# Kernel optimization log

Hardware: AMD Instinct MI355X
Metric: run time of the kernel (lower is better)

Reference implementation:

```python
import math
import jax, jax.numpy as jnp
import numpy as np

# Gemma4Audio config constants
HID = 1024
H = 8
D = HID // H            # 128
CHUNK = 12              # attention_chunk_size
PAST = 13 - 1           # max_past_horizon = context_left - 1
FUT = 0                 # max_future_horizon = context_right
CTX = CHUNK + PAST + FUT  # 24
SOFTCAP = 50.0
Q_SCALE = D ** (-0.5) / math.log(2)
K_SCALE = math.log(1.0 + math.e) / math.log(2)


def setup_inputs() -> dict:
    key = jax.random.key(0)
    ks = jax.random.split(key, 8)
    B, S = 4, 6144
    P = CTX + 1  # 25 relative positions
    std = HID ** (-0.5)
    return {
        "hidden_states": jax.random.normal(ks[0], (B, S, HID), jnp.float32),
        "position_embeddings": jax.random.normal(ks[1], (P, HID), jnp.float32),
        "Wq": jax.random.normal(ks[2], (HID, HID), jnp.float32) * std,
        "Wk": jax.random.normal(ks[3], (HID, HID), jnp.float32) * std,
        "Wv": jax.random.normal(ks[4], (HID, HID), jnp.float32) * std,
        "Wpost": jax.random.normal(ks[5], (HID, HID), jnp.float32) * std,
        "Wrel": jax.random.normal(ks[6], (HID, HID), jnp.float32) * std,
        "per_dim_scale": jnp.zeros((D,), jnp.float32),  # torch init: zeros
    }


def _extract_block_context(x, num_blocks):
    # x: [B, S, H, D] -> [B, num_blocks, CTX, H, D]
    xp = jnp.pad(x, ((0, 0), (PAST, FUT + CHUNK - 1), (0, 0), (0, 0)))
    idx = jnp.arange(num_blocks)[:, None] * CHUNK + jnp.arange(CTX)[None, :]
    return xp[:, idx]  # gather along seq axis


def _rel_shift(x):
    # x: [B, H, nb, CHUNK, P] -> [B, H, nb, CHUNK, CTX]
    B, Hh, nb, bs, pos_len = x.shape
    x = jnp.pad(x, ((0, 0), (0, 0), (0, 0), (0, 0), (0, CTX + 1 - pos_len)))
    x = x.reshape(B, Hh, nb, bs * (CTX + 1))[..., : bs * CTX]
    return x.reshape(B, Hh, nb, bs, CTX)


def reference(hidden_states, position_embeddings, Wq, Wk, Wv, Wpost, Wrel, per_dim_scale):
    B, S, _ = hidden_states.shape
    nb = (S + CHUNK - 1) // CHUNK
    pad = nb * CHUNK - S

    # Projections (ClippableLinear clamps are +/-inf at init -> identity)
    q = (hidden_states @ Wq.T).reshape(B, S, H, D)
    k = (hidden_states @ Wk.T).reshape(B, S, H, D)
    v = (hidden_states @ Wv.T).reshape(B, S, H, D)

    q = q * (Q_SCALE * jax.nn.softplus(per_dim_scale))  # per-dim scaled queries
    k = k * K_SCALE

    # [B, nb, CHUNK, H, D]
    q_blocked = jnp.pad(q, ((0, 0), (0, pad), (0, 0), (0, 0))).reshape(B, nb, CHUNK, H, D)
    k_ctx = _extract_block_context(k, nb)  # [B, nb, CTX, H, D]
    v_ctx = _extract_block_context(v, nb)

    # content score: [B, H, nb, CHUNK, CTX]
    matrix_ac = jnp.einsum('bnchd,bnkhd->bhnck', q_blocked, k_ctx)

    # relative position score
    rel_k = (position_embeddings @ Wrel.T).reshape(-1, H, D)  # [P, H, D]
    matrix_bd = jnp.einsum('bnchd,phd->bhncp', q_blocked, rel_k)
    matrix_bd = _rel_shift(matrix_bd)  # [B, H, nb, CHUNK, CTX]

    logits = matrix_ac + matrix_bd
    logits = jnp.tanh(logits / SOFTCAP) * SOFTCAP  # softcap
    attn = jax.nn.softmax(logits, axis=-1)

    out = jnp.einsum('bhnck,bnkhd->bnchd', attn, v_ctx)
    out = out.reshape(B, nb * CHUNK, H * D)[:, :S]
    return out @ Wpost.T
```

## Files before the change

kernel.cpp:

```cpp
#include <hip/hip_runtime.h>
#include <hip/hip_bf16.h>
#include <math.h>

typedef unsigned short ushort_t;
typedef __attribute__((ext_vector_type(8))) short short8;
typedef __attribute__((ext_vector_type(4))) short s4v;
typedef __attribute__((ext_vector_type(4))) float float4v;

#define HID 1024
#define NH 8
#define DH 128
#define CHUNK 12
#define PAST 12
#define CTX 24
#define NPOS 25
#define QKVW 3072

__device__ __forceinline__ float bf2f(ushort_t b){
  union{unsigned int u; float f;} x; x.u = ((unsigned int)b)<<16; return x.f;
}
__device__ __forceinline__ ushort_t f2bf(float f){
  union{float f; unsigned int u;} x; x.f = f;
  unsigned int u = x.u;
  unsigned int r = u + 0x7fffu + ((u>>16)&1u);
  return (ushort_t)(r>>16);
}

__device__ __forceinline__ void gload16(const ushort_t* g, ushort_t* l){
  __builtin_amdgcn_global_load_lds(
      (const __attribute__((address_space(1))) unsigned int*)g,
      (__attribute__((address_space(3))) unsigned int*)l,
      16, 0, 0);
}

__global__ __launch_bounds__(256) void cvt_all(
    const float* __restrict__ hs, const float* __restrict__ Wq,
    const float* __restrict__ Wk, const float* __restrict__ Wv,
    const float* __restrict__ Wp, ushort_t* __restrict__ hsb,
    ushort_t* __restrict__ Wcat, ushort_t* __restrict__ Wpb, int nhs4)
{
  const int W4 = 262144;
  const int total = nhs4 + 4*W4;
  for (int i = blockIdx.x*256 + threadIdx.x; i < total; i += gridDim.x*256){
    const float4v* src; s4v* dst; int off;
    if (i < nhs4){ src = (const float4v*)hs; dst = (s4v*)hsb; off = i; }
    else {
      int j = i - nhs4; int seg = j >> 18; off = j & (W4-1);
      src = (const float4v*)(seg==0?Wq:seg==1?Wk:seg==2?Wv:Wp);
      dst = (seg<3) ? ((s4v*)Wcat) + (size_t)seg*W4 : (s4v*)Wpb;
    }
    float4v v = src[off];
    s4v o;
#pragma unroll
    for (int j2=0;j2<4;j2++) o[j2] = (short)f2bf(v[j2]);
    dst[off] = o;
  }
}

template<int MODE, int OUTF>
__global__ __launch_bounds__(256) void gemm3(
    const ushort_t* __restrict__ A, const ushort_t* __restrict__ W,
    void* __restrict__ Cv, int M, int N, int K,
    const float* __restrict__ pds, float qsc, float ksc)
{
  const int nwg  = gridDim.x;
  const int orig = blockIdx.x;
  const int qch  = nwg >> 3, rch = nwg & 7;
  const int xcd  = orig & 7, idx = orig >> 3;
  const int bid  = (xcd < rch ? xcd*(qch+1) : rch*(qch+1) + (xcd-rch)*qch) + idx;

  const int NT = N >> 7;
  const int m0 = (bid / NT) * 128;
  const int n0 = (bid % NT) * 128;

  const int tid  = threadIdx.x;
  const int w    = tid >> 6, lane = tid & 63;
  const int wm   = w >> 1, wn = w & 1;
  const int lr   = lane & 15;
  const int lg   = lane >> 4;

  __shared__ ushort_t slab[6*128*32];
  ushort_t* a0 = slab;                 ushort_t* b0 = slab + 128*32;
  ushort_t* a1 = slab + 2*128*32;      ushort_t* b1 = slab + 3*128*32;
  ushort_t* a2 = slab + 4*128*32;      ushort_t* b2 = slab + 5*128*32;

  float4v acc[4][4];
#pragma unroll
  for (int i=0;i<4;i++)
#pragma unroll
    for (int j=0;j<4;j++) acc[i][j] = (float4v)0.0f;

  const int sr = lane >> 2;
  const int sc = (lane & 3) * 8;

  const ushort_t* Ab0 = A + (size_t)(m0 + w*16      + sr)*K + sc;
  const ushort_t* Ab1 = A + (size_t)(m0 + 64 + w*16 + sr)*K + sc;
  const ushort_t* Bb0 = W + (size_t)(n0 + w*16      + sr)*K + sc;
  const ushort_t* Bb1 = W + (size_t)(n0 + 64 + w*16 + sr)*K + sc;

#define STAGE(Abuf, Bbuf, kt) do {                    \
    gload16(Ab0 + (kt), &(Abuf)[(w*16)*32]);          \
    gload16(Ab1 + (kt), &(Abuf)[(64 + w*16)*32]);     \
    gload16(Bb0 + (kt), &(Bbuf)[(w*16)*32]);          \
    gload16(Bb1 + (kt), &(Bbuf)[(64 + w*16)*32]);     \
  } while(0)

#define COMPUTE(Abuf, Bbuf) do {                                             \
    short8 afr[4], bfr[4];                                                   \
    _Pragma("unroll")                                                        \
    for (int i=0;i<4;i++) afr[i] = *(const short8*)&(Abuf)[(wm*64 + i*16 + lr)*32 + lg*8]; \
    _Pragma("unroll")                                                        \
    for (int j=0;j<4;j++) bfr[j] = *(const short8*)&(Bbuf)[(wn*64 + j*16 + lr)*32 + lg*8]; \
    __builtin_amdgcn_s_setprio(1);                                           \
    _Pragma("unroll")                                                        \
    for (int i=0;i<4;i++)                                                    \
      _Pragma("unroll")                                                      \
      for (int j=0;j<4;j++)                                                  \
        acc[i][j] = __builtin_amdgcn_mfma_f32_16x16x32_bf16(afr[i], bfr[j], acc[i][j], 0,0,0); \
    __builtin_amdgcn_s_setprio(0);                                           \
  } while(0)

  const int nt = K >> 5;
  STAGE(a0, b0, 0);
  STAGE(a1, b1, 32);

  for (int t = 0; t < nt; ++t){
    if (t == nt-1) asm volatile("s_waitcnt vmcnt(0)" ::: "memory");
    else           asm volatile("s_waitcnt vmcnt(4)" ::: "memory");
    asm volatile("s_barrier" ::: "memory");
    if (t+2 < nt) STAGE(a2, b2, (t+2)*32);
    COMPUTE(a0, b0);
    ushort_t* ta = a0; a0 = a1; a1 = a2; a2 = ta;
    ushort_t* tb = b0; b0 = b1; b1 = b2; b2 = tb;
  }
#undef STAGE
#undef COMPUTE

  __syncthreads();

  if (OUTF == 0){
#pragma unroll
    for (int j=0;j<4;j++){
      const int col = wn*64 + j*16 + lr;
      float scale = 1.0f;
      if (MODE==1){
        const int gcol = n0 + col;
        if (gcol < 1024){ float p = pds[gcol & (DH-1)]; scale = qsc * log1pf(expf(p)); }
        else if (gcol < 2048) scale = ksc;
      }
#pragma unroll
      for (int i=0;i<4;i++){
        const int row = wm*64 + i*16 + lg*4;
#pragma unroll
        for (int r=0;r<4;r++)
          slab[(row + r)*128 + col] = f2bf(acc[i][j][r] * scale);
      }
    }
    __syncthreads();
    ushort_t* Crow = (ushort_t*)Cv + (size_t)m0*N + n0;
    const int rr = tid >> 4, sl = (tid & 15)*8;
#pragma unroll
    for (int it=0; it<8; ++it){
      const int row = it*16 + rr;
      *(short8*)&Crow[(size_t)row*N + sl] = *(const short8*)&slab[row*128 + sl];
    }
  } else {
    float* smf = (float*)slab;
    float* Crow = (float*)Cv + (size_t)m0*N + n0;
#pragma unroll
    for (int h2=0; h2<2; ++h2){
      __syncthreads();
      if (wm == h2){
#pragma unroll
        for (int j=0;j<4;j++){
          const int col = wn*64 + j*16 + lr;
#pragma unroll
          for (int i=0;i<4;i++){
            const int row = i*16 + lg*4;
#pragma unroll
            for (int r=0;r<4;r++)
              smf[(row + r)*128 + col] = acc[i][j][r];
          }
        }
      }
      __syncthreads();
      const int rr = tid >> 5, half = ((tid >> 4) & 1)*64, sl = (tid & 15)*4;
#pragma unroll
      for (int it=0; it<8; ++it){
        const int row = it*8 + rr;
        *(float4v*)&Crow[(size_t)(h2*64 + row)*N + half + sl] =
            *(const float4v*)&smf[row*128 + half + sl];
      }
    }
  }
}

__global__ __launch_bounds__(256) void relk2(
    const float* __restrict__ pe, const float* __restrict__ Wrel,
    ushort_t* __restrict__ rel)
{
  int g = blockIdx.x*256 + threadIdx.x;
  int idx = g >> 1, par = g & 1;
  if (idx >= NPOS*HID) return;
  int p = idx >> 10, n = idx & 1023;
  const float* a = pe + p*HID + par*512;
  const float* w = Wrel + (size_t)n*HID + par*512;
  float s = 0.f;
  for (int k=0;k<512;k+=4){
    float4v av = *(const float4v*)(a+k);
    float4v wv = *(const float4v*)(w+k);
#pragma unroll
    for (int u=0;u<4;u++) s += av[u]*wv[u];
  }
  s += __shfl_xor(s, 1, 64);
  if (!par) rel[idx] = f2bf(s);
}

__global__ __launch_bounds__(256) void attn_kernel(
  const ushort_t* __restrict__ qkv, const ushort_t* __restrict__ rel,
  ushort_t* __restrict__ o, int S)
{
  const int n0 = blockIdx.x * 4;
  const int b  = blockIdx.y, h = blockIdx.z;
  const int tid = threadIdx.x;
  const size_t bS = (size_t)b * S;

  __shared__ ushort_t lds[24800];
  ushort_t* ks = lds;
  ushort_t* vt = lds + 9248;
  float*    sB = (float*)(lds + 17952);
  ushort_t* rs = lds + 20448;
  float*    sA = (float*)(lds + 20448);

  const int base = n0*CHUNK - PAST;
  {
    const int r0 = tid >> 4;
    const int c0 = (tid & 15) * 8;
    for (int r = r0; r < 68; r += 16){
      int s = base + r;
      short8 kv = (short8)0, vv = (short8)0;
      if (r < 60 && s >= 0 && s < S){
        kv = *(const short8*)&qkv[(bS + s)*QKVW + 1024 + h*DH + c0];
        vv = *(const short8*)&qkv[(bS + s)*QKVW + 2048 + h*DH + c0];
      }
      *(short8*)&ks[r*136 + c0] = kv;
#pragma unroll
      for (int u=0;u<8;u++) vt[(c0+u)*68 + r] = (ushort_t)vv[u];
    }
    for (int r = r0; r < 32; r += 16){
      short8 rv = (short8)0;
      if (r < NPOS) rv = *(const short8*)&rel[r*HID + h*DH + c0];
      *(short8*)&rs[r*136 + c0] = rv;
    }
  }
  __syncthreads();

  const int w    = tid >> 6;
  const int lane = tid & 63;
  const int lr   = lane & 15;
  const int lg   = lane >> 4;

  float*    sAw = sA + w*312;
  float*    sBw = sB + w*312;
  ushort_t* Ppw = lds + w*640;

  int qrow = (n0 + w)*CHUNK + lr;
  if (qrow >= S) qrow = S - 1;
  const ushort_t* qp = qkv + (bS + qrow)*QKVW + h*DH + lg*8;
  short8 qf[4];
#pragma unroll
  for (int ks2=0; ks2<4; ks2++) qf[ks2] = *(const short8*)(qp + ks2*32);

#pragma unroll
  for (int t0=0; t0<2; t0++){
    float4v acc = (float4v)0.0f;
#pragma unroll
    for (int ks2=0; ks2<4; ks2++){
      short8 rf = *(const short8*)&rs[(t0*16 + lr)*136 + ks2*32 + lg*8];
      acc = __builtin_amdgcn_mfma_f32_16x16x32_bf16(qf[ks2], rf, acc, 0,0,0);
    }
    const int p = t0*16 + lr;
#pragma unroll
    for (int reg=0; reg<4; reg++){
      int cr = lg*4 + reg;
      if (cr < CHUNK && p < NPOS) sBw[cr*26 + p] = acc[reg];
    }
  }
  __syncthreads();

#pragma unroll
  for (int t0=0; t0<2; t0++){
    float4v acc = (float4v)0.0f;
#pragma unroll
    for (int ks2=0; ks2<4; ks2++){
      short8 kf = *(const short8*)&ks[(w*CHUNK + t0*16 + lr)*136 + ks2*32 + lg*8];
      acc = __builtin_amdgcn_mfma_f32_16x16x32_bf16(qf[ks2], kf, acc, 0,0,0);
    }
    const int t = t0*16 + lr;
#pragma unroll
    for (int reg=0; reg<4; reg++){
      int cr = lg*4 + reg;
      if (cr < CHUNK && t < CTX) sAw[cr*26 + t] = acc[reg];
    }
  }
  __syncthreads();

  if (lane < CHUNK) *(short8*)&Ppw[lane*40 + 24] = (short8)0;

  {
    const int c2 = lane >> 5;
    const int t  = lane & 31;
#pragma unroll
    for (int i=0;i<6;i++){
      int c = i*2 + c2;
      float x = -1e30f;
      if (t < CTX){
        int f = c*CTX + t;
        int r = f / NPOS, p = f - r*NPOS;
        x = sAw[c*26 + t] + sBw[r*26 + p];
        x = 50.0f * tanhf(x * 0.02f);
      }
      float m = x;
      for (int off=16; off>=1; off>>=1) m = fmaxf(m, __shfl_xor(m, off, 32));
      float e = (t < CTX) ? expf(x - m) : 0.0f;
      float s = e;
      for (int off=16; off>=1; off>>=1) s += __shfl_xor(s, off, 32);
      if (t < CTX) Ppw[c*40 + t] = f2bf(e / s);
    }
  }

  short8 pf = *(const short8*)&Ppw[lr*40 + lg*8];
  const int orow_base = (n0 + w)*CHUNK;
#pragma unroll
  for (int j=0; j<8; j++){
    int d  = j*16 + lr;
    int tb = w*CHUNK + lg*8;
    s4v b0 = *(const s4v*)&vt[d*68 + tb];
    s4v b1 = *(const s4v*)&vt[d*68 + tb + 4];
    short8 bf;
#pragma unroll
    for (int u=0;u<4;u++){ bf[u] = b0[u]; bf[u+4] = b1[u]; }
    float4v a = __builtin_amdgcn_mfma_f32_16x16x32_bf16(pf, bf, (float4v)0.0f, 0,0,0);
#pragma unroll
    for (int reg=0; reg<4; reg++){
      int cr = lg*4 + reg;
      if (cr < CHUNK)
        o[(bS + orow_base + cr)*HID + h*DH + j*16 + lr] = f2bf(a[reg]);
    }
  }
}

extern "C" void kernel_launch(void* const* d_in, const int* in_sizes, int n_in,
                              void* d_out, int out_size, void* d_ws, size_t ws_size,
                              hipStream_t stream)
{
  const float* hs    = (const float*)d_in[0];
  const float* pe    = (const float*)d_in[1];
  const float* Wq    = (const float*)d_in[2];
  const float* Wk    = (const float*)d_in[3];
  const float* Wv    = (const float*)d_in[4];
  const float* Wpost = (const float*)d_in[5];
  const float* Wrel  = (const float*)d_in[6];
  const float* pds   = (const float*)d_in[7];
  float* out = (float*)d_out;

  const int BS = in_sizes[0] / HID;
  const int B  = 4;
  const int S  = BS / B;
  const int nb = S / CHUNK;

  const size_t per = (size_t)BS * HID;
  const size_t wsz = (size_t)HID * HID;
  ushort_t* qkv  = (ushort_t*)d_ws;
  ushort_t* at   = qkv  + (size_t)BS * QKVW;
  ushort_t* rel  = at   + per;
  ushort_t* hsb  = rel  + (size_t)NPOS*HID;
  ushort_t* Wcat = hsb  + per;
  ushort_t* Wpb  = Wcat + 3*wsz;

  const float qsc = (float)(pow((double)DH, -0.5) / log(2.0));
  const float ksc = (float)(log(1.0 + exp(1.0)) / log(2.0));

  cvt_all<<<4096, 256, 0, stream>>>(hs, Wq, Wk, Wv, Wpost, hsb, Wcat, Wpb,
                                    (int)(per/4));
  relk2<<<200, 256, 0, stream>>>(pe, Wrel, rel);

  gemm3<1,0><<<(BS/128)*(QKVW/128), 256, 0, stream>>>(
      hsb, Wcat, qkv, BS, QKVW, HID, pds, qsc, ksc);
  attn_kernel<<<dim3(nb/4, B, NH), 256, 0, stream>>>(qkv, rel, at, S);
  gemm3<0,1><<<(BS/128)*(HID/128), 256, 0, stream>>>(
      at, Wpb, out, BS, HID, HID, nullptr, 1.0f, 1.0f);
}
```

Before: 386.6 us.

## Switch GEMM to 32x32x16 MFMA with XOR-swizzled LDS layout

Replaces the 4x4 grid of 16x16x32 bf16 MFMAs per wave with a 2x2 grid of 32x32x16 MFMAs, split into two K-halves per 32-wide tile. This cuts the number of LDS fragment reads and MFMA instructions per tile. It also XOR-swizzles the column offset used when staging global loads into shared memory and when reading fragments back, to reduce LDS bank conflicts. The epilogue is rewritten to match the 32x32 accumulator register layout, which makes the per-lane row mapping more complex.

```diff
diff --git a/kernel.cpp b/kernel.cpp
--- a/kernel.cpp
+++ b/kernel.cpp
@@ -6,6 +6,7 @@
 typedef __attribute__((ext_vector_type(8))) short short8;
 typedef __attribute__((ext_vector_type(4))) short s4v;
 typedef __attribute__((ext_vector_type(4))) float float4v;
+typedef __attribute__((ext_vector_type(16))) float f32x16;
 
 #define HID 1024
 #define NH 8
@@ -76,22 +77,30 @@
   const int tid  = threadIdx.x;
   const int w    = tid >> 6, lane = tid & 63;
   const int wm   = w >> 1, wn = w & 1;
-  const int lr   = lane & 15;
-  const int lg   = lane >> 4;
+  const int rl   = lane & 31;
+  const int sh   = lane >> 5;
+  const int xr   = (rl >> 1) & 3;
 
   __shared__ ushort_t slab[6*128*32];
   ushort_t* a0 = slab;                 ushort_t* b0 = slab + 128*32;
   ushort_t* a1 = slab + 2*128*32;      ushort_t* b1 = slab + 3*128*32;
   ushort_t* a2 = slab + 4*128*32;      ushort_t* b2 = slab + 5*128*32;
 
-  float4v acc[4][4];
-#pragma unroll
-  for (int i=0;i<4;i++)
-#pragma unroll
-    for (int j=0;j<4;j++) acc[i][j] = (float4v)0.0f;
+  f32x16 acc[2][2];
+#pragma unroll
+  for (int i=0;i<2;i++)
+#pragma unroll
+    for (int j=0;j<2;j++) acc[i][j] = (f32x16)0.0f;
 
   const int sr = lane >> 2;
-  const int sc = (lane & 3) * 8;
+  const int sc = ((lane & 3) ^ ((lane >> 3) & 3)) * 8;
+
+  const int ps0 = ((0*2 + sh) ^ xr) * 8;
+  const int ps1 = ((1*2 + sh) ^ xr) * 8;
+  const int aR0 = (wm*64      + rl)*32;
+  const int aR1 = (wm*64 + 32 + rl)*32;
+  const int bR0 = (wn*64      + rl)*32;
+  const int bR1 = (wn*64 + 32 + rl)*32;
 
   const ushort_t* Ab0 = A + (size_t)(m0 + w*16      + sr)*K + sc;
   const ushort_t* Ab1 = A + (size_t)(m0 + 64 + w*16 + sr)*K + sc;
@@ -106,17 +115,25 @@
   } while(0)
 
 #define COMPUTE(Abuf, Bbuf) do {                                             \
-    short8 afr[4], bfr[4];                                                   \
-    _Pragma("unroll")                                                        \
-    for (int i=0;i<4;i++) afr[i] = *(const short8*)&(Abuf)[(wm*64 + i*16 + lr)*32 + lg*8]; \
-    _Pragma("unroll")                                                        \
-    for (int j=0;j<4;j++) bfr[j] = *(const short8*)&(Bbuf)[(wn*64 + j*16 + lr)*32 + lg*8]; \
+    short8 fa0 = *(const short8*)&(Abuf)[aR0 + ps0];                         \
+    short8 fa1 = *(const short8*)&(Abuf)[aR1 + ps0];                         \
+    short8 fb0 = *(const short8*)&(Bbuf)[bR0 + ps0];                         \
+    short8 fb1 = *(const short8*)&(Bbuf)[bR1 + ps0];                         \
     __builtin_amdgcn_s_setprio(1);                                           \
-    _Pragma("unroll")                                                        \
-    for (int i=0;i<4;i++)                                                    \
-      _Pragma("unroll")                                                      \
-      for (int j=0;j<4;j++)                                                  \
-        acc[i][j] = __builtin_amdgcn_mfma_f32_16x16x32_bf16(afr[i], bfr[j], acc[i][j], 0,0,0); \
+    acc[0][0] = __builtin_amdgcn_mfma_f32_32x32x16_bf16(fa0, fb0, acc[0][0], 0,0,0); \
+    acc[0][1] = __builtin_amdgcn_mfma_f32_32x32x16_bf16(fa0, fb1, acc[0][1], 0,0,0); \
+    acc[1][0] = __builtin_amdgcn_mfma_f32_32x32x16_bf16(fa1, fb0, acc[1][0], 0,0,0); \
+    acc[1][1] = __builtin_amdgcn_mfma_f32_32x32x16_bf16(fa1, fb1, acc[1][1], 0,0,0); \
+    __builtin_amdgcn_s_setprio(0);                                           \
+    short8 ga0 = *(const short8*)&(Abuf)[aR0 + ps1];                         \
+    short8 ga1 = *(const short8*)&(Abuf)[aR1 + ps1];                         \
+    short8 gb0 = *(const short8*)&(Bbuf)[bR0 + ps1];                         \
+    short8 gb1 = *(const short8*)&(Bbuf)[bR1 + ps1];                         \
+    __builtin_amdgcn_s_setprio(1);                                           \
+    acc[0][0] = __builtin_amdgcn_mfma_f32_32x32x16_bf16(ga0, gb0, acc[0][0], 0,0,0); \
+    acc[0][1] = __builtin_amdgcn_mfma_f32_32x32x16_bf16(ga0, gb1, acc[0][1], 0,0,0); \
+    acc[1][0] = __builtin_amdgcn_mfma_f32_32x32x16_bf16(ga1, gb0, acc[1][0], 0,0,0); \
+    acc[1][1] = __builtin_amdgcn_mfma_f32_32x32x16_bf16(ga1, gb1, acc[1][1], 0,0,0); \
     __builtin_amdgcn_s_setprio(0);                                           \
   } while(0)
 
@@ -140,8 +157,8 @@
 
   if (OUTF == 0){
 #pragma unroll
-    for (int j=0;j<4;j++){
-      const int col = wn*64 + j*16 + lr;
+    for (int nj=0; nj<2; nj++){
+      const int col = wn*64 + nj*32 + rl;
       float scale = 1.0f;
       if (MODE==1){
         const int gcol = n0 + col;
@@ -149,11 +166,12 @@
         else if (gcol < 2048) scale = ksc;
       }
 #pragma unroll
-      for (int i=0;i<4;i++){
-        const int row = wm*64 + i*16 + lg*4;
-#pragma unroll
-        for (int r=0;r<4;r++)
-          slab[(row + r)*128 + col] = f2bf(acc[i][j][r] * scale);
+      for (int mi=0; mi<2; mi++){
+#pragma unroll
+        for (int reg=0; reg<16; reg++){
+          const int row = wm*64 + mi*32 + (reg&3) + 8*(reg>>2) + 4*sh;
+          slab[row*128 + col] = f2bf(acc[mi][nj][reg] * scale);
+        }
       }
     }
     __syncthreads();
@@ -172,14 +190,15 @@
       __syncthreads();
       if (wm == h2){
 #pragma unroll
-        for (int j=0;j<4;j++){
-          const int col = wn*64 + j*16 + lr;
-#pragma unroll
-          for (int i=0;i<4;i++){
-            const int row = i*16 + lg*4;
-#pragma unroll
-            for (int r=0;r<4;r++)
-              smf[(row + r)*128 + col] = acc[i][j][r];
+        for (int nj=0; nj<2; nj++){
+          const int col = wn*64 + nj*32 + rl;
+#pragma unroll
+          for (int mi=0; mi<2; mi++){
+#pragma unroll
+            for (int reg=0; reg<16; reg++){
+              const int lrow = mi*32 + (reg&3) + 8*(reg>>2) + 4*sh;
+              smf[lrow*128 + col] = acc[mi][nj][reg];
+            }
           }
         }
       }
```

Result: slower. 399.6 us (+3.4%).
